# Performance work log

Measured on AMD Instinct MI355X. Metric: run time of the kernel, lower is better.

## Reference

```python
import jax, jax.numpy as jnp
import numpy as np

B, C, H, W = 32, 256, 32, 32


def conv1x1(x, Wt, b):
    # x: [b,c,h,w], Wt: [out,in], b: [out] -- 1x1 conv == channel matmul
    return jnp.einsum('bchw,oc->bohw', x, Wt) + b[None, :, None, None]


def attn_logits(x, Wq, bq, Wk, bk):
    q = conv1x1(x, Wq, bq)
    k = conv1x1(x, Wk, bk)
    b, c, h, w = q.shape
    q = q.reshape(b, c, h * w)  # b c N
    k = k.reshape(b, c, h * w)
    # torch: q -> b (hw) c, k -> b c (hw); einsum bij,bjk->bik == q^T k over c
    return jnp.einsum('bci,bcj->bij', q, k) * (c ** -0.5)  # [b, N, N]


def setup_inputs() -> dict:
    key = jax.random.key(0)
    ks = jax.random.split(key, 8)
    s = 0.02
    return {
        'x1': jax.random.normal(ks[0], (B, C, H, W), jnp.float32),
        'x2': jax.random.normal(ks[1], (B, C, H, W), jnp.float32),
        'Wq': jax.random.normal(ks[2], (C, C), jnp.float32) * s,
        'bq': jnp.zeros((C,), jnp.float32),
        'Wk': jax.random.normal(ks[3], (C, C), jnp.float32) * s,
        'bk': jnp.zeros((C,), jnp.float32),
        'Wv': jax.random.normal(ks[4], (C, C), jnp.float32) * s,
        'bv': jnp.zeros((C,), jnp.float32),
        'Wps': jax.random.normal(ks[5], (C, C), jnp.float32) * s,
        'bps': jnp.zeros((C,), jnp.float32),
        'Wpc': jax.random.normal(ks[6], (C, C), jnp.float32) * s,
        'bpc': jnp.zeros((C,), jnp.float32),
    }


def reference(x1, x2, Wq, bq, Wk, bk, Wv, bv, Wps, bps, Wpc, bpc):
    b, c, h, w = x1.shape
    N = h * w
    # shared Attention module (same q/k weights for x1 and x2)
    w1 = attn_logits(x1, Wq, bq, Wk, bk)  # [b, N, N]
    w2 = attn_logits(x2, Wq, bq, Wk, bk)  # [b, N, N]
    v = conv1x1(x1, Wv, bv).reshape(b, c, N)  # [b, c, N]

    # self-attention branch: softmax over key dim (axis 2)
    a1 = jax.nn.softmax(w1, axis=2)
    # torch: h_[b,c,k] = sum_n v[b,c,n] * a1[b,k,n]
    h1 = jnp.einsum('bcn,bkn->bck', v, a1).reshape(b, c, h, w)
    h1 = conv1x1(h1, Wps, bps)

    # cross-attention branch: fused logits w1 + w2
    a12 = jax.nn.softmax(w1 + w2, axis=2)
    h12 = jnp.einsum('bcn,bkn->bck', v, a12).reshape(b, c, h, w)
    h12 = conv1x1(h12, Wpc, bpc)

    return (x1 + h1, x1 + h12)
```

## Files before the change

### kernel.cpp

```cpp
#include <hip/hip_runtime.h>


typedef unsigned short u16;
typedef __attribute__((ext_vector_type(8))) short bf16x8;
typedef __attribute__((ext_vector_type(4))) float f32x4;

#define MFMA16(a, b, c) __builtin_amdgcn_mfma_f32_16x16x32_bf16((a), (b), (c), 0, 0, 0)

#define NC 262144ull
#define REG 8388608ull
#define OFF_X1T  0ull
#define OFF_X2T  (REG)
#define OFF_Q1T  (2ull*REG)
#define OFF_K1T  (3ull*REG)
#define OFF_Q2T  (4ull*REG)
#define OFF_K2T  (5ull*REG)
#define OFF_V    (6ull*REG)
#define OFF_H1T  OFF_X1T
#define OFF_H12T OFF_X2T
#define WS_NEED_BYTES (7ull*REG*2)

__device__ __align__(16) u16 g_wb[5][65536];

__device__ __forceinline__ float b2f(u16 u) {
    union { unsigned int i; float f; } v; v.i = ((unsigned int)u) << 16; return v.f;
}
__device__ __forceinline__ u16 f2b(float f) {
    union { float f; unsigned int i; } v; v.f = f;
    unsigned int r = (v.i + 0x7FFFu + ((v.i >> 16) & 1u)) >> 16;
    return (u16)r;
}

__device__ __forceinline__ void gload16(const u16* g, u16* l) {
    __builtin_amdgcn_global_load_lds(
        (const __attribute__((address_space(1))) void*)g,
        (__attribute__((address_space(3))) void*)l,
        16, 0, 0);
}

__global__ void ksig(float* out, float val) {
    if (threadIdx.x == 0 && blockIdx.x == 0) out[0] = val;
}

__global__ __launch_bounds__(256) void kprep(
    const float* __restrict__ Wq, const float* __restrict__ Wk,
    const float* __restrict__ Wv, const float* __restrict__ Wps,
    const float* __restrict__ Wpc)
{
    int blk = blockIdx.x;
    int w = blk >> 6, j = blk & 63;
    const float* src = (w == 0) ? Wq : (w == 1) ? Wk : (w == 2) ? Wv : (w == 3) ? Wps : Wpc;
    int idx = j * 1024 + threadIdx.x * 4;
    float4 v = *(const float4*)(src + idx);
    ushort4 o;
    o.x = f2b(v.x); o.y = f2b(v.y); o.z = f2b(v.z); o.w = f2b(v.w);
    *(ushort4*)&g_wb[w][idx] = o;
}

__global__ __launch_bounds__(256) void ktrans(
    const float* __restrict__ x1, const float* __restrict__ x2, u16* __restrict__ ws)
{
    int nt = blockIdx.x, ct = blockIdx.y, bz = blockIdx.z;
    int b = bz >> 1, which = bz & 1;
    const float* X = (which ? x2 : x1) + (size_t)b * NC;
    u16* XT = ws + (which ? OFF_X2T : OFF_X1T) + (size_t)b * NC;
    int c0 = ct * 64, n0 = nt * 64;

    __shared__ __align__(16) u16 tile[64][68];
    int t = threadIdx.x;
    int tn = t & 15, tc = t >> 4;
#pragma unroll
    for (int j = 0; j < 4; ++j) {
        float4 v = *(const float4*)(X + (size_t)(c0 + 4 * tc + j) * 1024 + n0 + 4 * tn);
        u16* d = &tile[4 * tc + j][4 * tn];
        d[0] = f2b(v.x); d[1] = f2b(v.y); d[2] = f2b(v.z); d[3] = f2b(v.w);
    }
    __syncthreads();
    int tcB = t & 15, tnB = t >> 4;
#pragma unroll
    for (int i = 0; i < 4; ++i) {
        ushort4 o;
        o.x = tile[4 * tcB + 0][4 * tnB + i];
        o.y = tile[4 * tcB + 1][4 * tnB + i];
        o.z = tile[4 * tcB + 2][4 * tnB + i];
        o.w = tile[4 * tcB + 3][4 * tnB + i];
        *(ushort4*)(XT + (size_t)(n0 + 4 * tnB + i) * 256 + c0 + 4 * tcB) = o;
    }
}

__device__ __forceinline__ void gemm_core(
    const u16* __restrict__ A, const u16* __restrict__ B,
    int m0, int n0,
    void* __restrict__ C, int ldc, int cF32,
    const float* __restrict__ bias, int biasPerRow,
    const float* __restrict__ addSrc, int clampH)
{
    __shared__ __align__(16) u16 As[128 * 40];
    __shared__ __align__(16) u16 Bs[128 * 40];
    int t = threadIdx.x;
    int lane = t & 63, wave = t >> 6;
    int wm = wave >> 1, wn = wave & 1;
    int col = lane & 15, quad = lane >> 4;

    f32x4 acc[4][4];
#pragma unroll
    for (int i = 0; i < 4; ++i)
#pragma unroll
        for (int j = 0; j < 4; ++j) acc[i][j] = f32x4{0.f, 0.f, 0.f, 0.f};

    int r1 = t >> 2, c1 = t & 3;
    int r2 = r1 + 64;

    for (int kt = 0; kt < 8; ++kt) {
        int k0 = kt * 32;
        __syncthreads();
        *(uint4*)&As[r1 * 40 + c1 * 8] = *(const uint4*)(A + (size_t)(m0 + r1) * 256 + k0 + c1 * 8);
        *(uint4*)&As[r2 * 40 + c1 * 8] = *(const uint4*)(A + (size_t)(m0 + r2) * 256 + k0 + c1 * 8);
        *(uint4*)&Bs[r1 * 40 + c1 * 8] = *(const uint4*)(B + (size_t)(n0 + r1) * 256 + k0 + c1 * 8);
        *(uint4*)&Bs[r2 * 40 + c1 * 8] = *(const uint4*)(B + (size_t)(n0 + r2) * 256 + k0 + c1 * 8);
        __syncthreads();

        bf16x8 af[4], bf[4];
#pragma unroll
        for (int mf = 0; mf < 4; ++mf)
            af[mf] = *(const bf16x8*)&As[(wm * 64 + mf * 16 + col) * 40 + quad * 8];
#pragma unroll
        for (int nf = 0; nf < 4; ++nf)
            bf[nf] = *(const bf16x8*)&Bs[(wn * 64 + nf * 16 + col) * 40 + quad * 8];
#pragma unroll
        for (int mf = 0; mf < 4; ++mf)
#pragma unroll
            for (int nf = 0; nf < 4; ++nf)
                acc[mf][nf] = MFMA16(af[mf], bf[nf], acc[mf][nf]);
    }

#pragma unroll
    for (int mf = 0; mf < 4; ++mf)
#pragma unroll
        for (int nf = 0; nf < 4; ++nf) {
            int gm = m0 + wm * 64 + mf * 16 + quad * 4;
            int gn = n0 + wn * 64 + nf * 16 + col;
            float bcol = biasPerRow ? 0.f : bias[gn];
#pragma unroll
            for (int r = 0; r < 4; ++r) {
                int row = gm + r;
                float hv = acc[mf][nf][r] + (biasPerRow ? bias[row] : bcol);
                if (clampH) hv = fminf(fmaxf(hv, -0.05f), 0.05f);
                size_t ci = (size_t)row * ldc + gn;
                float v = hv + (addSrc ? addSrc[ci] : 0.f);
                if (cF32) ((float*)C)[ci] = v;
                else ((u16*)C)[ci] = f2b(v);
            }
        }
}

__global__ __launch_bounds__(256) void kproj(
    const float* __restrict__ bq, const float* __restrict__ bk,
    const float* __restrict__ bv, u16* __restrict__ ws)
{
    int blk = blockIdx.x;
    int xcd = blk & 7, jj = blk >> 3;
    int bg = jj / 80, id = jj % 80;
    int b = bg * 8 + xcd;
    const u16* X1T = ws + OFF_X1T + (size_t)b * NC;
    const u16* X2T = ws + OFF_X2T + (size_t)b * NC;
    if (id < 64) {
        int out = id >> 4, tt = id & 15, mt = tt >> 1, nt = tt & 1;
        const u16* A = (out < 2) ? X1T : X2T;
        const u16* W = (out & 1) ? &g_wb[1][0] : &g_wb[0][0];
        const float* bb = (out & 1) ? bk : bq;
        size_t off = (out == 0) ? OFF_Q1T : (out == 1) ? OFF_K1T : (out == 2) ? OFF_Q2T : OFF_K2T;
        u16* C = ws + off + (size_t)b * NC;
        gemm_core(A, W, mt * 128, nt * 128, C, 256, 0, bb, 0, nullptr, 0);
    } else {
        int tt = id - 64, mt = tt >> 3, nt = tt & 7;
        u16* C = ws + OFF_V + (size_t)b * NC;
        gemm_core(&g_wb[2][0], X1T, mt * 128, nt * 128, C, 1024, 0, bv, 1, nullptr, 0);
    }
}

__global__ __launch_bounds__(512, 2) void kattn(u16* __restrict__ ws)
{
    int blk = blockIdx.x;
    int xcd = blk & 7, jj = blk >> 3;
    int b = ((jj >> 3) << 3) + xcd;
    int qt = jj & 7;
    int t = threadIdx.x, lane = t & 63, wave = t >> 6;
    int col = lane & 15, quad = lane >> 4;

    const u16* Q1T = ws + OFF_Q1T + (size_t)b * NC;
    const u16* K1T = ws + OFF_K1T + (size_t)b * NC;
    const u16* Q2T = ws + OFF_Q2T + (size_t)b * NC;
    const u16* K2T = ws + OFF_K2T + (size_t)b * NC;
    const u16* V   = ws + OFF_V   + (size_t)b * NC;
    u16* H1T  = ws + OFF_H1T  + (size_t)b * NC;
    u16* H12T = ws + OFF_H12T + (size_t)b * NC;

    __shared__ __align__(16) u16 K1s[2][8192];
    __shared__ __align__(16) u16 K2s[2][8192];
    __shared__ __align__(16) u16 Vs[2][8192];
    __shared__ __align__(16) u16 Ps[8][16 * 36];

    int i0 = qt * 128 + wave * 16;

    bf16x8 aq1[8], aq2[8];
#pragma unroll
    for (int f = 0; f < 8; ++f) {
        aq1[f] = *(const bf16x8*)(Q1T + (size_t)(i0 + col) * 256 + f * 32 + quad * 8);
        aq2[f] = *(const bf16x8*)(Q2T + (size_t)(i0 + col) * 256 + f * 32 + quad * 8);
    }

    f32x4 h1[16], h12[16];
#pragma unroll
    for (int cf = 0; cf < 16; ++cf) { h1[cf] = f32x4{0.f,0.f,0.f,0.f}; h12[cf] = f32x4{0.f,0.f,0.f,0.f}; }
    float l1p[4], l2p[4];
#pragma unroll
    for (int r = 0; r < 4; ++r) { l1p[r] = 0.f; l2p[r] = 0.f; }

    const float sc = 0.0901684400555602f;
    const float SH = 5.770780163555851f;

    int kr_ = t >> 5;
    int kwb = (t & 31) << 4;
    int kwl = kwb ^ ((kr_ & 7) << 4);
    const u16* k1src = K1T + (size_t)kr_ * 256 + (kwl >> 1);
    const u16* k2src = K2T + (size_t)kr_ * 256 + (kwl >> 1);
    int vrow = t >> 2;
    int vo = (t & 3) << 3;
    const u16* vsrc = V + (size_t)vrow * 1024 + vo;
    int ldsw = wave * 512;

    gload16(k1src,          &K1s[0][ldsw]);
    gload16(k1src + 4096,   &K1s[0][ldsw + 4096]);
    gload16(k2src,          &K2s[0][ldsw]);
    gload16(k2src + 4096,   &K2s[0][ldsw + 4096]);
    gload16(vsrc,           &Vs[0][ldsw]);
    gload16(vsrc + 131072,  &Vs[0][ldsw + 4096]);

    u16* P = Ps[wave];
    int swz = (col & 7) << 3;

    for (int it = 0; it < 32; ++it) {
        int cur = it & 1;
        __syncthreads();

        if (it < 31) {
            int nxt = cur ^ 1;
            const u16* s1 = k1src + (size_t)(it + 1) * 8192;
            const u16* s2 = k2src + (size_t)(it + 1) * 8192;
            const u16* sv = vsrc + (size_t)(it + 1) * 32;
            gload16(s1,          &K1s[nxt][ldsw]);
            gload16(s1 + 4096,   &K1s[nxt][ldsw + 4096]);
            gload16(s2,          &K2s[nxt][ldsw]);
            gload16(s2 + 4096,   &K2s[nxt][ldsw + 4096]);
            gload16(sv,          &Vs[nxt][ldsw]);
            gload16(sv + 131072, &Vs[nxt][ldsw + 4096]);
        }

        const u16* K1c = K1s[cur];
        const u16* K2c = K2s[cur];
        const u16* Vc  = Vs[cur];

        f32x4 s1v[2], s2v[2];
        s1v[0] = s1v[1] = s2v[0] = s2v[1] = f32x4{0.f,0.f,0.f,0.f};
        __builtin_amdgcn_s_setprio(1);
#pragma unroll
        for (int nf = 0; nf < 2; ++nf) {
            int krow = nf * 16 + col;
#pragma unroll
            for (int f = 0; f < 8; ++f) {
                int wb = (f * 32 + quad * 8) ^ swz;
                bf16x8 bk1 = *(const bf16x8*)&K1c[krow * 256 + wb];
                s1v[nf] = MFMA16(aq1[f], bk1, s1v[nf]);
                bf16x8 bk2 = *(const bf16x8*)&K2c[krow * 256 + wb];
                s2v[nf] = MFMA16(aq2[f], bk2, s2v[nf]);
            }
        }
        __builtin_amdgcn_s_setprio(0);

#pragma unroll
        for (int r = 0; r < 4; ++r) {
            float p0 = __builtin_amdgcn_exp2f(s1v[0][r] * sc - SH);
            float p1 = __builtin_amdgcn_exp2f(s1v[1][r] * sc - SH);
            l1p[r] += p0 + p1;
            P[(quad * 4 + r) * 36 + col] = f2b(p0);
            P[(quad * 4 + r) * 36 + 16 + col] = f2b(p1);
        }
        bf16x8 p1f = *(const bf16x8*)&P[col * 36 + quad * 8];

#pragma unroll
        for (int r = 0; r < 4; ++r) {
            float s0 = s1v[0][r] + s2v[0][r];
            float s1x = s1v[1][r] + s2v[1][r];
            float p0 = __builtin_amdgcn_exp2f(s0 * sc - SH);
            float p1 = __builtin_amdgcn_exp2f(s1x * sc - SH);
            l2p[r] += p0 + p1;
            P[(quad * 4 + r) * 36 + col] = f2b(p0);
            P[(quad * 4 + r) * 36 + 16 + col] = f2b(p1);
        }
        bf16x8 p2f = *(const bf16x8*)&P[col * 36 + quad * 8];

        __builtin_amdgcn_s_setprio(1);
#pragma unroll
        for (int cf = 0; cf < 16; ++cf) {
            bf16x8 bv = *(const bf16x8*)&Vc[(cf * 16 + col) * 32 + quad * 8];
            h1[cf] = MFMA16(p1f, bv, h1[cf]);
            h12[cf] = MFMA16(p2f, bv, h12[cf]);
        }
        __builtin_amdgcn_s_setprio(0);
    }

    float inv1[4], inv2[4];
#pragma unroll
    for (int r = 0; r < 4; ++r) {
        float s = l1p[r];
        s += __shfl_xor(s, 1); s += __shfl_xor(s, 2);
        s += __shfl_xor(s, 4); s += __shfl_xor(s, 8);
        inv1[r] = 1.f / s;
        float s2x = l2p[r];
        s2x += __shfl_xor(s2x, 1); s2x += __shfl_xor(s2x, 2);
        s2x += __shfl_xor(s2x, 4); s2x += __shfl_xor(s2x, 8);
        inv2[r] = 1.f / s2x;
    }
#pragma unroll
    for (int cf = 0; cf < 16; ++cf)
#pragma unroll
        for (int r = 0; r < 4; ++r) {
            size_t addr = (size_t)(i0 + quad * 4 + r) * 256 + cf * 16 + col;
            H1T[addr] = f2b(h1[cf][r] * inv1[r]);
            H12T[addr] = f2b(h12[cf][r] * inv2[r]);
        }
}

__global__ __launch_bounds__(256) void kfinal(
    const float* __restrict__ x1,
    const float* __restrict__ bps, const float* __restrict__ bpc,
    const u16* __restrict__ ws, float* __restrict__ out)
{
    int blk = blockIdx.x;
    int xcd = blk & 7, jj = blk >> 3;
    int b = ((jj >> 5) << 3) + xcd;
    int rest = jj & 31;
    int br = rest >> 4, id = rest & 15;
    int mt = id >> 3, nt = id & 7;
    const u16* H = ws + (br ? OFF_H12T : OFF_H1T) + (size_t)b * NC;
    const u16* W = br ? &g_wb[4][0] : &g_wb[3][0];
    const float* bb = br ? bpc : bps;
    const float* X = x1 + (size_t)b * NC;
    float* C = out + (size_t)br * REG + (size_t)b * NC;
    gemm_core(W, H, mt * 128, nt * 128, C, 1024, 1, bb, 1, X, 1);
}

extern "C" void kernel_launch(void* const* d_in, const int* in_sizes, int n_in,
                              void* d_out, int out_size, void* d_ws, size_t ws_size,
                              hipStream_t stream)
{
    float* out = (float*)d_out;
    u16* ws = (u16*)d_ws;

    if (ws_size < WS_NEED_BYTES) { ksig<<<1, 64, 0, stream>>>(out, 1.0e7f); return; }
    if (n_in != 12 || in_sizes[0] != 8388608 || in_sizes[1] != 8388608 ||
        in_sizes[2] != 65536 || in_sizes[3] != 256 || out_size != 16777216) {
        ksig<<<1, 64, 0, stream>>>(out, 5.0e6f); return;
    }

    const float* x1  = (const float*)d_in[0];
    const float* x2  = (const float*)d_in[1];
    const float* Wq  = (const float*)d_in[2];
    const float* bq  = (const float*)d_in[3];
    const float* Wk  = (const float*)d_in[4];
    const float* bk  = (const float*)d_in[5];
    const float* Wv  = (const float*)d_in[6];
    const float* bv  = (const float*)d_in[7];
    const float* Wps = (const float*)d_in[8];
    const float* bps = (const float*)d_in[9];
    const float* Wpc = (const float*)d_in[10];
    const float* bpc = (const float*)d_in[11];

    kprep<<<320, 256, 0, stream>>>(Wq, Wk, Wv, Wps, Wpc);
    ktrans<<<dim3(16, 4, 64), 256, 0, stream>>>(x1, x2, ws);
    kproj<<<2560, 256, 0, stream>>>(bq, bk, bv, ws);
    kattn<<<256, 512, 0, stream>>>(ws);
    kfinal<<<1024, 256, 0, stream>>>(x1, bps, bpc, ws, out);
}
```

Before: 342.9 us.

## Double-buffer GEMM LDS tiles with direct global-to-LDS loads and swizzle

Replaces the padded single-buffer LDS staging in the shared GEMM core with two ping-pong buffers filled by direct global-to-LDS loads. The loads for the next K-slice are issued before the current slice's MFMAs, which drops one barrier per iteration and overlaps memory with compute. An XOR swizzle on the 16-byte chunk index replaces the row padding to avoid LDS bank conflicts. MFMA priority is raised around the math block. It relies on the barrier also waiting for the outstanding async LDS writes, and it doubles LDS use per block, which may lower occupancy.

```diff
diff --git a/kernel.cpp b/kernel.cpp
--- a/kernel.cpp
+++ b/kernel.cpp
@@ -95,8 +95,8 @@
     const float* __restrict__ bias, int biasPerRow,
     const float* __restrict__ addSrc, int clampH)
 {
-    __shared__ __align__(16) u16 As[128 * 40];
-    __shared__ __align__(16) u16 Bs[128 * 40];
+    __shared__ __align__(16) u16 As[2][4096];
+    __shared__ __align__(16) u16 Bs[2][4096];
     int t = threadIdx.x;
     int lane = t & 63, wave = t >> 6;
     int wm = wave >> 1, wn = wave & 1;
@@ -108,30 +108,44 @@
 #pragma unroll
         for (int j = 0; j < 4; ++j) acc[i][j] = f32x4{0.f, 0.f, 0.f, 0.f};
 
-    int r1 = t >> 2, c1 = t & 3;
-    int r2 = r1 + 64;
+    int rA = t >> 2;
+    int lA = (((t & 3) ^ ((t >> 3) & 3)) << 3);
+    const u16* aB = A + (size_t)(m0 + rA) * 256 + lA;
+    const u16* bB = B + (size_t)(n0 + rA) * 256 + lA;
+    int ldsw = wave * 512;
+
+    int rchunk = ((quad ^ ((col >> 1) & 3)) << 3);
+
+    gload16(aB,          &As[0][ldsw]);
+    gload16(aB + 16384,  &As[0][ldsw + 2048]);
+    gload16(bB,          &Bs[0][ldsw]);
+    gload16(bB + 16384,  &Bs[0][ldsw + 2048]);
 
     for (int kt = 0; kt < 8; ++kt) {
-        int k0 = kt * 32;
+        int cur = kt & 1;
         __syncthreads();
-        *(uint4*)&As[r1 * 40 + c1 * 8] = *(const uint4*)(A + (size_t)(m0 + r1) * 256 + k0 + c1 * 8);
-        *(uint4*)&As[r2 * 40 + c1 * 8] = *(const uint4*)(A + (size_t)(m0 + r2) * 256 + k0 + c1 * 8);
-        *(uint4*)&Bs[r1 * 40 + c1 * 8] = *(const uint4*)(B + (size_t)(n0 + r1) * 256 + k0 + c1 * 8);
-        *(uint4*)&Bs[r2 * 40 + c1 * 8] = *(const uint4*)(B + (size_t)(n0 + r2) * 256 + k0 + c1 * 8);
-        __syncthreads();
+        if (kt < 7) {
+            int off = (kt + 1) * 32;
+            gload16(aB + off,          &As[cur ^ 1][ldsw]);
+            gload16(aB + off + 16384,  &As[cur ^ 1][ldsw + 2048]);
+            gload16(bB + off,          &Bs[cur ^ 1][ldsw]);
+            gload16(bB + off + 16384,  &Bs[cur ^ 1][ldsw + 2048]);
+        }
 
         bf16x8 af[4], bf[4];
 #pragma unroll
         for (int mf = 0; mf < 4; ++mf)
-            af[mf] = *(const bf16x8*)&As[(wm * 64 + mf * 16 + col) * 40 + quad * 8];
+            af[mf] = *(const bf16x8*)&As[cur][(wm * 64 + mf * 16 + col) * 32 + rchunk];
 #pragma unroll
         for (int nf = 0; nf < 4; ++nf)
-            bf[nf] = *(const bf16x8*)&Bs[(wn * 64 + nf * 16 + col) * 40 + quad * 8];
+            bf[nf] = *(const bf16x8*)&Bs[cur][(wn * 64 + nf * 16 + col) * 32 + rchunk];
+        __builtin_amdgcn_s_setprio(1);
 #pragma unroll
         for (int mf = 0; mf < 4; ++mf)
 #pragma unroll
             for (int nf = 0; nf < 4; ++nf)
                 acc[mf][nf] = MFMA16(af[mf], bf[nf], acc[mf][nf]);
+        __builtin_amdgcn_s_setprio(0);
     }
 
 #pragma unroll
```

After: 328.7 us. 4.1% less time.
